# Optimization experiments

Hardware: AMD Instinct MI355X
Metric: run time of the kernel (lower is better)

## Reference

```python
import jax, jax.numpy as jnp
import numpy as np

N = 1024   # chain length n
B = 4      # bond_dim (forced by eye(4) bias in original)
P = 2      # phys_dim
BS = 8     # batch size


def setup_inputs() -> dict:
    key = jax.random.key(0)
    k1, k2, k3 = jax.random.split(key, 3)
    data = jax.random.randint(k1, (BS, N), 0, 2).astype(jnp.float32)
    # near-identity init (identity + small noise), as in the original (std*randn + eye bias),
    # but with std large enough to be numerically non-trivial yet stable over ~n matmuls
    eye_b = jnp.eye(B, dtype=jnp.float32)[:, :, None]            # (B, B, 1) broadcast over phys
    tri_up = 0.01 * jax.random.normal(k2, ((N - 1) * N // 2, B, B, P), jnp.float32) + eye_b
    diag = 0.01 * jax.random.normal(k3, (N, B, P), jnp.float32) + 1.0
    return {"data": data, "tri_up": tri_up, "diag": diag}


def reference(data, tri_up, diag):
    bs, n = data.shape
    b = tri_up.shape[1]
    p = tri_up.shape[3]
    emb = jnp.stack([data, 1.0 - data], axis=2)                  # (bs, n, p)
    # scatter tri_up into lower triangle (incl. diagonal) of (n-1, n-1) grid
    r, c = jnp.tril_indices(n - 1)
    T = jnp.zeros((n - 1, n - 1, b, b, p), tri_up.dtype).at[r, c].set(tri_up)
    # contract physical index with embedded spins of sites 0..n-2; output axes swapped to (m, n, bs, b, b)
    T = jnp.einsum('nmlri,bmi->mnblr', T, emb[:, :-1])           # (n-1, n-1, bs, b, b)
    # strict lower triangle (m > n) -> identity matrices
    ru, cu = jnp.triu_indices(n - 1, k=1)
    T = T.at[cu, ru].set(jnp.eye(b, dtype=T.dtype))
    # binary-tree contraction along axis 0 (recursive doubling of 4x4 matmuls)
    size = T.shape[0]
    while size > 1:
        half = size // 2
        nice = 2 * half
        leftover = T[nice:]
        T = jnp.einsum('mnbik,mnbkj->mnbij', T[0:nice:2], T[1:nice:2])
        T = jnp.concatenate([T, leftover], axis=0)
        size = half + (size % 2)
    T = T[0][..., 0, :]                                          # (n-1, bs, b): first row of each matrix
    out = jnp.einsum('nbd,ndp->nbp', T, diag[1:])                # (n-1, bs, p)
    first = jnp.broadcast_to(diag[0, 0], out[0].shape)[None]     # (1, bs, p)
    out = jnp.concatenate([first, out], axis=0)                  # (n, bs, p)
    logx = jax.nn.log_softmax(out, axis=-1).transpose(1, 0, 2)   # (bs, n, p)
    log_prob = logx[:, :, 0] * data + logx[:, :, 1] * (1.0 - data)
    return log_prob.sum(-1)                                      # (bs,)
```

## Files before the change

### kernel.cpp

```cpp
#include <hip/hip_runtime.h>


#define NPOS   1024
#define SEGLEN 128
#define MAXSEG 8
#define CH     8
#define NBUF   4
#define NWAVE  2300
#define TRI_ELEMS (523776 * 32)

template<int l>
__device__ __forceinline__ float qb(float x) {
    constexpr int ctrl = l * 0x55;
    return __int_as_float(__builtin_amdgcn_update_dpp(
        __float_as_int(x), __float_as_int(x), ctrl, 0xF, 0xF, false));
}
template<int ctrl>
__device__ __forceinline__ float qperm(float x) {
    return __int_as_float(__builtin_amdgcn_update_dpp(
        __float_as_int(x), __float_as_int(x), ctrl, 0xF, 0xF, false));
}

__device__ __forceinline__ void gl_lds16(const float* g, float* l) {
    __builtin_amdgcn_global_load_lds(
        (const __attribute__((address_space(1))) void*)g,
        (__attribute__((address_space(3))) void*)l, 16, 0, 0);
}

#define WAITVM(N) __builtin_amdgcn_s_waitcnt((N) | 0x0F70)

__device__ __forceinline__ void decode_task(int id, int& s, int& n) {
    int base = 0, cnt = 1023;
    s = 0;
    while (id >= base + cnt) { base += cnt; s++; cnt -= 128; }
    n = 1022 - (id - base);
}

__global__ __launch_bounds__(64) void amps_seg(
        const float* __restrict__ data,
        const float* __restrict__ tri,
        float* __restrict__ segout)
{
    const int lane = threadIdx.x;
    const int w    = blockIdx.x;
    const int t    = lane >> 5;
    const int q    = lane & 31;
    const int b    = q >> 2;
    const int i    = q & 3;

    int sA, nA, sB, nB;
    decode_task(2 * w,     sA, nA);
    decode_task(2 * w + 1, sB, nB);
    const int g0A = sA * SEGLEN,            g0B = sB * SEGLEN;
    const int stepsA = min(SEGLEN, nA + 1 - g0A);
    const int stepsB = min(SEGLEN, nB + 1 - g0B);
    const int tstA = (nA * (nA + 1) / 2 + g0A) * 32;
    const int tstB = (nB * (nB + 1) / 2 + g0B) * 32;

    const int nchA = (stepsA >> 3) + ((stepsA & 7) ? 1 : 0);
    const int nchB = (stepsB >> 3) + ((stepsB & 7) ? 1 : 0);
    const int nch  = max(nchA, nchB);

    const int g0_my    = t ? g0B : g0A;
    const int steps_my = t ? stepsB : stepsA;
    const int chunkf   = steps_my >> 3;
    const int rem      = steps_my & 7;
    const int n_my     = t ? nB : nA;
    const int s_my     = t ? sB : sA;

    __shared__ float lds[2][NBUF * CH * 32];

    unsigned m0, m1, m2, m3;
    {
        const float4* dp4 =
            (const float4*)(data + b * NPOS + g0_my + i * 32);
        float4 f[8];
        #pragma unroll
        for (int u = 0; u < 8; u++) f[u] = dp4[u];
        unsigned piece = 0;
        #pragma unroll
        for (int u = 0; u < 8; u++) {
            piece |= (f[u].x != 1.0f) ? (1u << (u * 4 + 0)) : 0u;
            piece |= (f[u].y != 1.0f) ? (1u << (u * 4 + 1)) : 0u;
            piece |= (f[u].z != 1.0f) ? (1u << (u * 4 + 2)) : 0u;
            piece |= (f[u].w != 1.0f) ? (1u << (u * 4 + 3)) : 0u;
        }
        m0 = (unsigned)__shfl((int)piece, t * 32 + b * 4 + 0);
        m1 = (unsigned)__shfl((int)piece, t * 32 + b * 4 + 1);
        m2 = (unsigned)__shfl((int)piece, t * 32 + b * 4 + 2);
        m3 = (unsigned)__shfl((int)piece, t * 32 + b * 4 + 3);
    }

    auto stageA = [&](int c) {
        int off = min(tstA + c * 256 + lane * 4, TRI_ELEMS - 4);
        gl_lds16(tri + off, &lds[0][(c & (NBUF - 1)) * 256]);
    };
    auto stageB = [&](int c) {
        int off = min(tstB + c * 256 + lane * 4, TRI_ELEMS - 4);
        gl_lds16(tri + off, &lds[1][(c & (NBUF - 1)) * 256]);
    };

    stageA(0); stageB(0);
    stageA(1); stageB(1);
    stageA(2); stageB(2);

    float* __restrict__ mybuf = &lds[t][0];

    float c0 = (i == 0) ? 1.0f : 0.0f;
    float c1 = (i == 1) ? 1.0f : 0.0f;
    float c2 = (i == 2) ? 1.0f : 0.0f;
    float c3 = (i == 3) ? 1.0f : 0.0f;

    const float idval = ((q >> 3) == ((q >> 1) & 3)) ? 1.0f : 0.0f;

    for (int c = 0; c < nch; c++) {
        stageA(c + 3); stageB(c + 3);
        WAITVM(6);

        if (c >= chunkf) {
            const int mstart = (c == chunkf) ? rem : 0;
            float* bp = mybuf + (c & (NBUF - 1)) * 256 + q;
            for (int m = mstart; m < CH; m++) bp[m * 32] = idval;
        }

        unsigned word = (c < 8) ? ((c < 4) ? m0 : m1) : ((c < 12) ? m2 : m3);
        const unsigned bits = (word >> ((c & 3) * 8)) & 0xFFu;
        const float* __restrict__ buf = mybuf + (c & (NBUF - 1)) * 256;

        #pragma unroll
        for (int m = 0; m < CH; m++) {
            const float* p = buf + m * 32 + ((bits >> m) & 1u);
            float n0 = fmaf(c3, p[24], fmaf(c2, p[16], fmaf(c1, p[8],  c0 * p[0])));
            float n1 = fmaf(c3, p[26], fmaf(c2, p[18], fmaf(c1, p[10], c0 * p[2])));
            float n2 = fmaf(c3, p[28], fmaf(c2, p[20], fmaf(c1, p[12], c0 * p[4])));
            float n3 = fmaf(c3, p[30], fmaf(c2, p[22], fmaf(c1, p[14], c0 * p[6])));
            c0 = n0; c1 = n1; c2 = n2; c3 = n3;
        }
    }

    const size_t o = (((size_t)n_my * MAXSEG + s_my) * 8 + b) * 16 + i;
    segout[o +  0] = c0;
    segout[o +  4] = c1;
    segout[o +  8] = c2;
    segout[o + 12] = c3;
}

__global__ __launch_bounds__(256) void amps_combine(
        const float* __restrict__ segout,
        const float* __restrict__ diag,
        const float* __restrict__ data,
        float* __restrict__ out)
{
    const int tid = threadIdx.x;
    const int q   = tid >> 5;
    const int sub = tid & 31;
    const int b   = sub >> 2;
    const int r   = sub & 3;
    const int n   = blockIdx.x * 8 + q;

    __shared__ float sh[64];

    float res = 0.0f;
    if (n < NPOS - 1) {
        const int nseg = n / SEGLEN + 1;
        const float* basep = segout + (size_t)n * (MAXSEG * 128)
                           + b * 16 + r * 4;
        float4 P[8];
        #pragma unroll
        for (int s2 = 0; s2 < 8; s2++)
            P[s2] = *(const float4*)(basep + s2 * 128);

        float v = (r == 0) ? 1.0f : 0.0f;
        #pragma unroll
        for (int s2 = 0; s2 < 8; s2++) {
            float acc = qb<0>(v) * P[s2].x;
            acc = fmaf(qb<1>(v), P[s2].y, acc);
            acc = fmaf(qb<2>(v), P[s2].z, acc);
            float vn = fmaf(qb<3>(v), P[s2].w, acc);
            v = (s2 < nseg) ? vn : v;
        }

        const int pos = n + 1;
        const float* dg = diag + pos * 8 + r * 2;
        float o0 = v * dg[0];
        float o1 = v * dg[1];
        o0 += qperm<0xB1>(o0); o0 += qperm<0x4E>(o0);
        o1 += qperm<0xB1>(o1); o1 += qperm<0x4E>(o1);
        float mx  = fmaxf(o0, o1);
        float lse = mx + __logf(__expf(o0 - mx) + __expf(o1 - mx));
        float dsel = data[b * NPOS + pos];
        res = ((dsel == 1.0f) ? o0 : o1) - lse;
    }
    if (r == 0) sh[q * 8 + b] = res;
    __syncthreads();
    if (tid < 8) {
        float ssum = 0.0f;
        #pragma unroll
        for (int qq = 0; qq < 8; qq++) ssum += sh[qq * 8 + tid];
        if (blockIdx.x == 0) {
            float o0 = diag[0], o1 = diag[1];
            float mx  = fmaxf(o0, o1);
            float lse = mx + __logf(__expf(o0 - mx) + __expf(o1 - mx));
            float d0  = data[tid * NPOS];
            ssum += ((d0 == 1.0f) ? o0 : o1) - lse;
        }
        atomicAdd(out + tid, ssum);
    }
}

extern "C" void kernel_launch(void* const* d_in, const int* in_sizes, int n_in,
                              void* d_out, int out_size, void* d_ws, size_t ws_size,
                              hipStream_t stream)
{
    const float* data = (const float*)d_in[0];
    const float* tri  = (const float*)d_in[1];
    const float* diag = (const float*)d_in[2];

    float* segout = (float*)d_ws;
    float* out    = (float*)d_out;

    hipMemsetAsync(d_out, 0, 8 * sizeof(float), stream);
    amps_seg<<<dim3(NWAVE), dim3(64), 0, stream>>>(data, tri, segout);
    amps_combine<<<dim3(128), dim3(256), 0, stream>>>(segout, diag, data, out);
}
```

Measured before the change: 118.9 us.

## Halve segment length, pack four waves per block, use DPP in chain matmul

Segment length drops from 128 to 64, which doubles the number of segment tasks (8688) and shortens each serial chain of 4x4 matmuls. The extra parallelism is meant to cut the critical-path latency of the kernel. Four waves now share one 256-thread block with separate LDS regions. The inner matmul reads one LDS value per row and broadcasts coefficients across lanes with DPP, which replaces 16 LDS reads per step. The main loop skips identity padding until the tail chunks, and the combine kernel reads segments on demand up to a variable count, at the cost of a longer serial combine over up to 16 segments.

```diff
diff --git a/kernel.cpp b/kernel.cpp
--- a/kernel.cpp
+++ b/kernel.cpp
@@ -2,11 +2,13 @@
 
 
 #define NPOS   1024
-#define SEGLEN 128
-#define MAXSEG 8
+#define SEGLEN 64
+#define MAXSEG 16
 #define CH     8
 #define NBUF   4
-#define NWAVE  2300
+#define NTASK  8688
+#define NWAVE  (NTASK / 2)
+#define NBLOCK (NWAVE / 4)
 #define TRI_ELEMS (523776 * 32)
 
 template<int l>
@@ -32,17 +34,19 @@
 __device__ __forceinline__ void decode_task(int id, int& s, int& n) {
     int base = 0, cnt = 1023;
     s = 0;
-    while (id >= base + cnt) { base += cnt; s++; cnt -= 128; }
+    while (id >= base + cnt) { base += cnt; s++; cnt -= SEGLEN; }
     n = 1022 - (id - base);
 }
 
-__global__ __launch_bounds__(64) void amps_seg(
+__global__ __launch_bounds__(256, 4) void amps_seg(
         const float* __restrict__ data,
         const float* __restrict__ tri,
         float* __restrict__ segout)
 {
-    const int lane = threadIdx.x;
-    const int w    = blockIdx.x;
+    const int tid  = threadIdx.x;
+    const int wid  = tid >> 6;
+    const int lane = tid & 63;
+    const int w    = blockIdx.x * 4 + wid;
     const int t    = lane >> 5;
     const int q    = lane & 31;
     const int b    = q >> 2;
@@ -57,9 +61,11 @@
     const int tstA = (nA * (nA + 1) / 2 + g0A) * 32;
     const int tstB = (nB * (nB + 1) / 2 + g0B) * 32;
 
-    const int nchA = (stepsA >> 3) + ((stepsA & 7) ? 1 : 0);
-    const int nchB = (stepsB >> 3) + ((stepsB & 7) ? 1 : 0);
-    const int nch  = max(nchA, nchB);
+    const int fullA = stepsA >> 3,          fullB = stepsB >> 3;
+    const int nchA = fullA + ((stepsA & 7) ? 1 : 0);
+    const int nchB = fullB + ((stepsB & 7) ? 1 : 0);
+    const int nch   = max(nchA, nchB);
+    const int mainc = min(fullA, fullB);
 
     const int g0_my    = t ? g0B : g0A;
     const int steps_my = t ? stepsB : stepsA;
@@ -68,74 +74,98 @@
     const int n_my     = t ? nB : nA;
     const int s_my     = t ? sB : sA;
 
-    __shared__ float lds[2][NBUF * CH * 32];
-
-    unsigned m0, m1, m2, m3;
+    __shared__ float lds_all[4][2][NBUF * CH * 32];
+    float* __restrict__ ldsA = &lds_all[wid][0][0];
+    float* __restrict__ ldsB = &lds_all[wid][1][0];
+
+    unsigned m0, m1;
     {
-        const float4* dp4 =
-            (const float4*)(data + b * NPOS + g0_my + i * 32);
-        float4 f[8];
-        #pragma unroll
-        for (int u = 0; u < 8; u++) f[u] = dp4[u];
+        const float4* dp4 = (const float4*)(data + b * NPOS + g0_my + i * 16);
+        float4 f0 = dp4[0], f1 = dp4[1], f2 = dp4[2], f3 = dp4[3];
         unsigned piece = 0;
-        #pragma unroll
-        for (int u = 0; u < 8; u++) {
-            piece |= (f[u].x != 1.0f) ? (1u << (u * 4 + 0)) : 0u;
-            piece |= (f[u].y != 1.0f) ? (1u << (u * 4 + 1)) : 0u;
-            piece |= (f[u].z != 1.0f) ? (1u << (u * 4 + 2)) : 0u;
-            piece |= (f[u].w != 1.0f) ? (1u << (u * 4 + 3)) : 0u;
-        }
-        m0 = (unsigned)__shfl((int)piece, t * 32 + b * 4 + 0);
-        m1 = (unsigned)__shfl((int)piece, t * 32 + b * 4 + 1);
-        m2 = (unsigned)__shfl((int)piece, t * 32 + b * 4 + 2);
-        m3 = (unsigned)__shfl((int)piece, t * 32 + b * 4 + 3);
+        piece |= (f0.x != 1.0f) ? 1u : 0;        piece |= (f0.y != 1.0f) ? 2u : 0;
+        piece |= (f0.z != 1.0f) ? 4u : 0;        piece |= (f0.w != 1.0f) ? 8u : 0;
+        piece |= (f1.x != 1.0f) ? 0x10u : 0;     piece |= (f1.y != 1.0f) ? 0x20u : 0;
+        piece |= (f1.z != 1.0f) ? 0x40u : 0;     piece |= (f1.w != 1.0f) ? 0x80u : 0;
+        piece |= (f2.x != 1.0f) ? 0x100u : 0;    piece |= (f2.y != 1.0f) ? 0x200u : 0;
+        piece |= (f2.z != 1.0f) ? 0x400u : 0;    piece |= (f2.w != 1.0f) ? 0x800u : 0;
+        piece |= (f3.x != 1.0f) ? 0x1000u : 0;   piece |= (f3.y != 1.0f) ? 0x2000u : 0;
+        piece |= (f3.z != 1.0f) ? 0x4000u : 0;   piece |= (f3.w != 1.0f) ? 0x8000u : 0;
+        const int sb = t * 32 + b * 4;
+        m0 = (unsigned)__shfl((int)piece, sb + 0)
+           | ((unsigned)__shfl((int)piece, sb + 1) << 16);
+        m1 = (unsigned)__shfl((int)piece, sb + 2)
+           | ((unsigned)__shfl((int)piece, sb + 3) << 16);
     }
 
     auto stageA = [&](int c) {
         int off = min(tstA + c * 256 + lane * 4, TRI_ELEMS - 4);
-        gl_lds16(tri + off, &lds[0][(c & (NBUF - 1)) * 256]);
+        gl_lds16(tri + off, ldsA + (c & (NBUF - 1)) * 256);
     };
     auto stageB = [&](int c) {
         int off = min(tstB + c * 256 + lane * 4, TRI_ELEMS - 4);
-        gl_lds16(tri + off, &lds[1][(c & (NBUF - 1)) * 256]);
+        gl_lds16(tri + off, ldsB + (c & (NBUF - 1)) * 256);
     };
 
     stageA(0); stageB(0);
     stageA(1); stageB(1);
     stageA(2); stageB(2);
 
-    float* __restrict__ mybuf = &lds[t][0];
+    float* __restrict__ mybuf = t ? ldsB : ldsA;
 
     float c0 = (i == 0) ? 1.0f : 0.0f;
     float c1 = (i == 1) ? 1.0f : 0.0f;
     float c2 = (i == 2) ? 1.0f : 0.0f;
     float c3 = (i == 3) ? 1.0f : 0.0f;
 
-    const float idval = ((q >> 3) == ((q >> 1) & 3)) ? 1.0f : 0.0f;
-
-    for (int c = 0; c < nch; c++) {
+    auto bits_of = [&](int c) -> unsigned {
+        unsigned word = (c < 4) ? m0 : m1;
+        return (word >> ((c & 3) * 8)) & 0xFFu;
+    };
+
+    auto compute = [&](int c) {
+        const unsigned bits = bits_of(c);
+        const float* __restrict__ buf = mybuf + (c & (NBUF - 1)) * 256 + i * 8;
+        #pragma unroll
+        for (int m = 0; m < CH; m++) {
+            const float* p = buf + m * 32 + ((bits >> m) & 1u);
+            float a0 = p[0], a1 = p[2], a2 = p[4], a3 = p[6];
+            float n0 = qb<0>(a0) * c0;
+            n0 = fmaf(qb<1>(a0), c1, n0);
+            n0 = fmaf(qb<2>(a0), c2, n0);
+            n0 = fmaf(qb<3>(a0), c3, n0);
+            float n1 = qb<0>(a1) * c0;
+            n1 = fmaf(qb<1>(a1), c1, n1);
+            n1 = fmaf(qb<2>(a1), c2, n1);
+            n1 = fmaf(qb<3>(a1), c3, n1);
+            float n2 = qb<0>(a2) * c0;
+            n2 = fmaf(qb<1>(a2), c1, n2);
+            n2 = fmaf(qb<2>(a2), c2, n2);
+            n2 = fmaf(qb<3>(a2), c3, n2);
+            float n3 = qb<0>(a3) * c0;
+            n3 = fmaf(qb<1>(a3), c1, n3);
+            n3 = fmaf(qb<2>(a3), c2, n3);
+            n3 = fmaf(qb<3>(a3), c3, n3);
+            c0 = n0; c1 = n1; c2 = n2; c3 = n3;
+        }
+    };
+
+    int c = 0;
+    for (; c < mainc; c++) {
         stageA(c + 3); stageB(c + 3);
         WAITVM(6);
-
+        compute(c);
+    }
+    const float idval = ((q >> 3) == ((q >> 1) & 3)) ? 1.0f : 0.0f;
+    for (; c < nch; c++) {
+        stageA(c + 3); stageB(c + 3);
+        WAITVM(6);
         if (c >= chunkf) {
             const int mstart = (c == chunkf) ? rem : 0;
             float* bp = mybuf + (c & (NBUF - 1)) * 256 + q;
             for (int m = mstart; m < CH; m++) bp[m * 32] = idval;
         }
-
-        unsigned word = (c < 8) ? ((c < 4) ? m0 : m1) : ((c < 12) ? m2 : m3);
-        const unsigned bits = (word >> ((c & 3) * 8)) & 0xFFu;
-        const float* __restrict__ buf = mybuf + (c & (NBUF - 1)) * 256;
-
-        #pragma unroll
-        for (int m = 0; m < CH; m++) {
-            const float* p = buf + m * 32 + ((bits >> m) & 1u);
-            float n0 = fmaf(c3, p[24], fmaf(c2, p[16], fmaf(c1, p[8],  c0 * p[0])));
-            float n1 = fmaf(c3, p[26], fmaf(c2, p[18], fmaf(c1, p[10], c0 * p[2])));
-            float n2 = fmaf(c3, p[28], fmaf(c2, p[20], fmaf(c1, p[12], c0 * p[4])));
-            float n3 = fmaf(c3, p[30], fmaf(c2, p[22], fmaf(c1, p[14], c0 * p[6])));
-            c0 = n0; c1 = n1; c2 = n2; c3 = n3;
-        }
+        compute(c);
     }
 
     const size_t o = (((size_t)n_my * MAXSEG + s_my) * 8 + b) * 16 + i;
@@ -165,19 +195,15 @@
         const int nseg = n / SEGLEN + 1;
         const float* basep = segout + (size_t)n * (MAXSEG * 128)
                            + b * 16 + r * 4;
-        float4 P[8];
-        #pragma unroll
-        for (int s2 = 0; s2 < 8; s2++)
-            P[s2] = *(const float4*)(basep + s2 * 128);
-
         float v = (r == 0) ? 1.0f : 0.0f;
         #pragma unroll
-        for (int s2 = 0; s2 < 8; s2++) {
-            float acc = qb<0>(v) * P[s2].x;
-            acc = fmaf(qb<1>(v), P[s2].y, acc);
-            acc = fmaf(qb<2>(v), P[s2].z, acc);
-            float vn = fmaf(qb<3>(v), P[s2].w, acc);
-            v = (s2 < nseg) ? vn : v;
+        for (int s2 = 0; s2 < MAXSEG; s2++) {
+            if (s2 >= nseg) break;
+            float4 P = *(const float4*)(basep + s2 * 128);
+            float acc = qb<0>(v) * P.x;
+            acc = fmaf(qb<1>(v), P.y, acc);
+            acc = fmaf(qb<2>(v), P.z, acc);
+            v   = fmaf(qb<3>(v), P.w, acc);
         }
 
         const int pos = n + 1;
@@ -220,6 +246,6 @@
     float* out    = (float*)d_out;
 
     hipMemsetAsync(d_out, 0, 8 * sizeof(float), stream);
-    amps_seg<<<dim3(NWAVE), dim3(64), 0, stream>>>(data, tri, segout);
+    amps_seg<<<dim3(NBLOCK), dim3(256), 0, stream>>>(data, tri, segout);
     amps_combine<<<dim3(128), dim3(256), 0, stream>>>(segout, diag, data, out);
 }
```

New measurement: 121.7 us. +2.3%, slower.
